# Kernel tuning notes

Measured on AMD Instinct MI355X. Metric: run time of the kernel, lower is better.

Reference implementation:

```python
import jax, jax.numpy as jnp
import numpy as np
import math

N_HEADS = 8
D_EMBED = 512
D_CROSS = 768
D_HEAD = D_EMBED // N_HEADS


def _conv1x1(w, b, t):
    # 1x1 conv == pointwise matmul over channel dim. t: [B, Cin, H, W], w: [Cout, Cin]
    out = jnp.einsum('oc,bchw->bohw', w, t)
    return out + b[None, :, None, None]


def setup_inputs() -> dict:
    key = jax.random.key(0)
    ks = jax.random.split(key, 10)
    s = 0.02
    return {
        'x': jax.random.normal(ks[0], (8, D_EMBED, 32, 32), dtype=jnp.float32),
        'y': jax.random.normal(ks[1], (8, D_CROSS, 32, 32), dtype=jnp.float32),
        'w_q': jax.random.normal(ks[2], (D_EMBED, D_EMBED), dtype=jnp.float32) * s,
        'b_q': jnp.zeros((D_EMBED,), dtype=jnp.float32),
        'w_k': jax.random.normal(ks[3], (D_EMBED, D_CROSS), dtype=jnp.float32) * s,
        'b_k': jnp.zeros((D_EMBED,), dtype=jnp.float32),
        'w_v': jax.random.normal(ks[4], (D_EMBED, D_CROSS), dtype=jnp.float32) * s,
        'b_v': jnp.zeros((D_EMBED,), dtype=jnp.float32),
        'w_o': jax.random.normal(ks[5], (D_EMBED, D_EMBED), dtype=jnp.float32) * s,
        'b_o': jnp.zeros((D_EMBED,), dtype=jnp.float32),
    }


def reference(x, y, w_q, b_q, w_k, b_k, w_v, b_v, w_o, b_o):
    B, C, H, W = x.shape
    N = H * W
    q = _conv1x1(w_q, b_q, x)  # [B, C, H, W]
    k = _conv1x1(w_k, b_k, y)
    v = _conv1x1(w_v, b_v, y)
    # flat reshape [B, C, H, W] -> [B, nH, d_head, N] (row-major, matches torch .view)
    q = q.reshape(B, N_HEADS, D_HEAD, N)
    k = k.reshape(B, N_HEADS, D_HEAD, N)
    v = v.reshape(B, N_HEADS, D_HEAD, N)
    # attn = q^T k / sqrt(d_head): [B, nH, N, N]
    scores = jnp.einsum('bhdq,bhdk->bhqk', q, k) / math.sqrt(D_HEAD)
    attn = jax.nn.softmax(scores, axis=-1)
    # out = attn @ v^T : [B, nH, N, d_head]
    out = jnp.einsum('bhqk,bhdk->bhqd', attn, v)
    # faithful quirk: flat reshape (no transpose back) to [B, C, H, W]
    out = out.reshape(B, N_HEADS * D_HEAD, H, W)
    return _conv1x1(w_o, b_o, out)
```

## Files before the change

### kernel.cpp

```cpp
#include <hip/hip_runtime.h>
#include <cstddef>
#include <cstdint>


typedef short bs8 __attribute__((ext_vector_type(8)));
typedef short bs4 __attribute__((ext_vector_type(4)));
typedef float fx4 __attribute__((ext_vector_type(4)));

#define MFMA16(a, b, c) __builtin_amdgcn_mfma_f32_16x16x32_bf16((a), (b), (c), 0, 0, 0)

#define GLOAD_LDS16(g, l)                                                  \
  __builtin_amdgcn_global_load_lds(                                        \
      (const __attribute__((address_space(1))) void*)(g),                  \
      (__attribute__((address_space(3))) void*)(l), 16, 0, 0)

__device__ __forceinline__ short f2b(float f) {
  unsigned u = __builtin_bit_cast(unsigned, f);
  u = (u + 0x7fff + ((u >> 16) & 1)) >> 16;
  return (short)u;
}

__device__ __forceinline__ unsigned cvt_pk_bf16(float lo, float hi) {
  unsigned r;
  asm("v_cvt_pk_bf16_f32 %0, %1, %2" : "=v"(r) : "v"(lo), "v"(hi));
  return r;
}

__device__ __forceinline__ float exp2_fast(float x) {
  float r;
  asm("v_exp_f32 %0, %1" : "=v"(r) : "v"(x));
  return r;
}

#define QSCALE 0.1803368801111244f

__global__ __launch_bounds__(256) void prep(
    const float* __restrict__ w_q, const float* __restrict__ w_k,
    const float* __restrict__ w_v, const float* __restrict__ w_o,
    short* __restrict__ wdst,
    const float* __restrict__ x, short* __restrict__ xt,
    const float* __restrict__ y, short* __restrict__ yt)
{
  __shared__ short T[64][72];
  const int bid = blockIdx.x;
  const int t = threadIdx.x;

  if (bid < 1280) {
    const int i = bid * 1024 + t * 4;
    const float* src; int off;
    if (i < 262144)       { src = w_q; off = 0; }
    else if (i < 655360)  { src = w_k; off = 262144; }
    else if (i < 1048576) { src = w_v; off = 655360; }
    else                  { src = w_o; off = 1048576; }
    float4 f = *(const float4*)(src + (i - off));
    bs4 o; o[0] = f2b(f.x); o[1] = f2b(f.y); o[2] = f2b(f.z); o[3] = f2b(f.w);
    *(bs4*)(wdst + i) = o;
    return;
  }

  const float* src; short* dst; int C, nt, ct, b;
  if (bid < 2304) {
    const int local = bid - 1280;
    src = x; dst = xt; C = 512;
    nt = local & 15; ct = (local >> 4) & 7; b = local >> 7;
  } else {
    const int local = bid - 2304;
    src = y; dst = yt; C = 768;
    nt = local & 15; const int rest = local >> 4; ct = rest % 12; b = rest / 12;
  }

  const size_t srcBase = ((size_t)b * C + ct * 64) * 1024 + nt * 64;
  #pragma unroll
  for (int p = 0; p < 4; ++p) {
    const int lin = p * 256 + t;
    const int row = lin >> 4;
    const int seg = lin & 15;
    float4 f = *(const float4*)(src + srcBase + (size_t)row * 1024 + seg * 4);
    T[seg * 4 + 0][row] = f2b(f.x);
    T[seg * 4 + 1][row] = f2b(f.y);
    T[seg * 4 + 2][row] = f2b(f.z);
    T[seg * 4 + 3][row] = f2b(f.w);
  }
  __syncthreads();
  const size_t dstBase = ((size_t)b * 1024 + nt * 64) * C + ct * 64;
  #pragma unroll
  for (int p = 0; p < 2; ++p) {
    const int lin = p * 256 + t;
    const int row = lin >> 3;
    const int seg = lin & 7;
    *(bs8*)(dst + dstBase + (size_t)row * C + seg * 8) = *(const bs8*)&T[row][seg * 8];
  }
}

__global__ __launch_bounds__(256) void tcast_b(
    const short* __restrict__ src, short* __restrict__ dst, int C)
{
  __shared__ short T[64][72];
  const int t = threadIdx.x;
  const int nt = blockIdx.x, ct = blockIdx.y, b = blockIdx.z;
  const size_t srcBase = ((size_t)b * C + ct * 64) * 1024 + nt * 64;
  #pragma unroll
  for (int p = 0; p < 4; ++p) {
    const int lin = p * 256 + t;
    const int row = lin >> 4;
    const int seg = lin & 15;
    bs4 v = *(const bs4*)(src + srcBase + (size_t)row * 1024 + seg * 4);
    #pragma unroll
    for (int j = 0; j < 4; ++j) T[seg * 4 + j][row] = v[j];
  }
  __syncthreads();
  const size_t dstBase = ((size_t)b * 1024 + nt * 64) * C + ct * 64;
  #pragma unroll
  for (int p = 0; p < 2; ++p) {
    const int lin = p * 256 + t;
    const int row = lin >> 3;
    const int seg = lin & 7;
    *(bs8*)(dst + dstBase + (size_t)row * C + seg * 8) = *(const bs8*)&T[row][seg * 8];
  }
}

template<int MODE, int MTL2>
__device__ __forceinline__ void gemm2_body(
    short* As0, short* As1, short* Bs0, short* Bs1, int hw, int tid,
    const short* __restrict__ W, const short* __restrict__ Xt,
    const float* __restrict__ bias, const float* __restrict__ bias2,
    void* __restrict__ Cout, void* __restrict__ Cout2, int K, float scale)
{
  const int wid = tid >> 6, l = tid & 63;
  const int swz = (hw & 7) * (8 << MTL2) + (hw >> 3);
  const int n0 = (swz & 7) * 128;
  const int m0 = ((swz >> 3) & ((1 << MTL2) - 1)) * 128;
  const int b  = swz >> (3 + MTL2);
  const int wm = wid >> 2, wn = wid & 3;

  const int lrow = l >> 3;
  const int swz8 = ((l & 7) ^ lrow) * 8;
  const int x7 = l & 7;

  const short* Wg = W + (size_t)m0 * K;
  const short* Xg = Xt + ((size_t)b * 1024 + n0) * K;

  fx4 acc[4][2] = {};
  const int NK = K >> 6;

  #pragma unroll
  for (int j = 0; j < 2; ++j) {
    const int rb = j * 64 + wid * 8;
    const int row = rb + lrow;
    GLOAD_LDS16(Wg + (size_t)row * K + swz8, As0 + rb * 64);
    GLOAD_LDS16(Xg + (size_t)row * K + swz8, Bs0 + rb * 64);
  }
  __syncthreads();

  auto gstep = [&](const short* AsC, const short* BsC, short* AsN, short* BsN,
                   int kn, bool pre) {
    if (pre) {
      #pragma unroll
      for (int j = 0; j < 2; ++j) {
        const int rb = j * 64 + wid * 8;
        const int row = rb + lrow;
        GLOAD_LDS16(Wg + (size_t)row * K + kn + swz8, AsN + rb * 64);
        GLOAD_LDS16(Xg + (size_t)row * K + kn + swz8, BsN + rb * 64);
      }
    }
    #pragma unroll
    for (int kb = 0; kb < 2; ++kb) {
      bs8 af[4], bfr[2];
      const int u = (kb * 4 + (l >> 4)) ^ x7;
      #pragma unroll
      for (int ms = 0; ms < 4; ++ms) {
        const int rr = wm * 64 + ms * 16 + (l & 15);
        af[ms] = *(const bs8*)&AsC[rr * 64 + u * 8];
      }
      #pragma unroll
      for (int ns = 0; ns < 2; ++ns) {
        const int rr = wn * 32 + ns * 16 + (l & 15);
        bfr[ns] = *(const bs8*)&BsC[rr * 64 + u * 8];
      }
      #pragma unroll
      for (int ms = 0; ms < 4; ++ms)
        #pragma unroll
        for (int ns = 0; ns < 2; ++ns)
          acc[ms][ns] = MFMA16(af[ms], bfr[ns], acc[ms][ns]);
    }
    __syncthreads();
  };

  const int NK2 = NK >> 1;
  for (int p = 0; p < NK2; ++p) {
    gstep(As0, Bs0, As1, Bs1, (2 * p + 1) * 64, true);
    gstep(As1, Bs1, As0, Bs0, (2 * p + 2) * 64, (2 * p + 2) < NK);
  }

  #pragma unroll
  for (int ms = 0; ms < 4; ++ms) {
    #pragma unroll
    for (int ns = 0; ns < 2; ++ns) {
      const int n = n0 + wn * 32 + ns * 16 + (l & 15);
      const int mb = m0 + wm * 64 + ms * 16 + (l >> 4) * 4;
      if (MODE == 0) {
        const float f0 = (acc[ms][ns][0] + bias[mb + 0]) * scale;
        const float f1 = (acc[ms][ns][1] + bias[mb + 1]) * scale;
        const float f2 = (acc[ms][ns][2] + bias[mb + 2]) * scale;
        const float f3 = (acc[ms][ns][3] + bias[mb + 3]) * scale;
        uint2 od; od.x = cvt_pk_bf16(f0, f1); od.y = cvt_pk_bf16(f2, f3);
        short* dst = (short*)Cout + (((size_t)b * 8 + (mb >> 6)) * 1024 + n) * 64 + (mb & 63);
        *(uint2*)dst = od;
      } else if (MODE == 2) {
        #pragma unroll
        for (int r = 0; r < 4; ++r)
          ((float*)Cout)[((size_t)b * 512 + mb + r) * 1024 + n] = acc[ms][ns][r] + bias[mb + r];
      } else {
        if (mb < 512) {
          const float f0 = acc[ms][ns][0] + bias[mb + 0];
          const float f1 = acc[ms][ns][1] + bias[mb + 1];
          const float f2 = acc[ms][ns][2] + bias[mb + 2];
          const float f3 = acc[ms][ns][3] + bias[mb + 3];
          uint2 od; od.x = cvt_pk_bf16(f0, f1); od.y = cvt_pk_bf16(f2, f3);
          short* dst = (short*)Cout + (((size_t)b * 8 + (mb >> 6)) * 1024 + n) * 64 + (mb & 63);
          *(uint2*)dst = od;
        } else {
          const int c = mb - 512;
          #pragma unroll
          for (int r = 0; r < 4; ++r)
            ((short*)Cout2)[((size_t)b * 512 + c + r) * 1024 + n] = f2b(acc[ms][ns][r] + bias2[c + r]);
        }
      }
    }
  }
}

__global__ __launch_bounds__(512) void gemm_qkv(
    const short* __restrict__ wq, const short* __restrict__ wkv,
    const short* __restrict__ xt, const short* __restrict__ yt,
    const float* __restrict__ b_q, const float* __restrict__ b_k,
    const float* __restrict__ b_v,
    short* __restrict__ Qw, short* __restrict__ Kw, short* __restrict__ Vw)
{
  __shared__ short As[2][128 * 64];
  __shared__ short Bs[2][128 * 64];
  if (blockIdx.x < 256)
    gemm2_body<0, 2>(As[0], As[1], Bs[0], Bs[1], blockIdx.x, threadIdx.x,
                     wq, xt, b_q, nullptr, (void*)Qw, nullptr, 512, QSCALE);
  else
    gemm2_body<3, 3>(As[0], As[1], Bs[0], Bs[1], blockIdx.x - 256, threadIdx.x,
                     wkv, yt, b_k, b_v, (void*)Kw, (void*)Vw, 768, 1.0f);
}

__global__ __launch_bounds__(512) void gemm_o(
    const short* __restrict__ wo, const short* __restrict__ Ot,
    const float* __restrict__ b_o, float* __restrict__ out)
{
  __shared__ short As[2][128 * 64];
  __shared__ short Bs[2][128 * 64];
  gemm2_body<2, 2>(As[0], As[1], Bs[0], Bs[1], blockIdx.x, threadIdx.x,
                   wo, Ot, b_o, nullptr, (void*)out, nullptr, 512, 1.0f);
}

__global__ __launch_bounds__(512) void attn_mfma(
    const short* __restrict__ Q, const short* __restrict__ Kt,
    const short* __restrict__ V, short* __restrict__ O)
{
  __shared__ short Ks[2][64 * 64];
  __shared__ short Vs[2][64 * 64];
  __shared__ short Ps[8][16 * 64];

  const int t = threadIdx.x, wid = t >> 6, l = t & 63;
  const int hw = blockIdx.x;
  const int swzb = (hw & 7) * 64 + (hw >> 3);
  const int qt = swzb & 7, h = (swzb >> 3) & 7, b = swzb >> 6;
  const int q0 = qt * 128 + wid * 16;
  const size_t bh = (size_t)b * 8 + h;

  const short* Qg = Q + (bh * 1024 + q0) * 64;
  const short* Kg = Kt + bh * 1024 * 64;
  const short* Vg = V + bh * 64 * 1024;

  const int g = l >> 4;
  const int q = l & 15;
  const int x7 = q & 7;
  const int lrow = l >> 3;
  const int swz8 = ((l & 7) ^ lrow) * 8;
  short* Pw = Ps[wid];

  const bs8 onesf = {0x3F80, 0x3F80, 0x3F80, 0x3F80, 0x3F80, 0x3F80, 0x3F80, 0x3F80};

  bs8 qf[2];
  #pragma unroll
  for (int db = 0; db < 2; ++db)
    qf[db] = *(const bs8*)(Qg + (size_t)q * 64 + db * 32 + g * 8);

  {
    const int row = wid * 8 + lrow;
    GLOAD_LDS16(Kg + (size_t)row * 64 + swz8, &Ks[0][wid * 8 * 64]);
    GLOAD_LDS16(Vg + (size_t)row * 1024 + swz8, &Vs[0][wid * 8 * 64]);
  }
  __syncthreads();

  fx4 oacc[4] = {};
  fx4 lacc = {};

  auto tile = [&](const short* KsC, const short* VsC, short* KsN, short* VsN,
                  int ktn, bool pre) {
    if (pre) {
      const int k0n = ktn * 64;
      const int row = wid * 8 + lrow;
      GLOAD_LDS16(Kg + (size_t)(k0n + row) * 64 + swz8, KsN + wid * 8 * 64);
      GLOAD_LDS16(Vg + (size_t)row * 1024 + k0n + swz8, VsN + wid * 8 * 64);
    }

    fx4 s[4] = {};
    __builtin_amdgcn_s_setprio(1);
    #pragma unroll
    for (int ks = 0; ks < 4; ++ks) {
      const int rr = ks * 16 + q;
      #pragma unroll
      for (int db = 0; db < 2; ++db) {
        bs8 kf = *(const bs8*)&KsC[rr * 64 + ((db * 4 + g) ^ x7) * 8];
        s[ks] = MFMA16(kf, qf[db], s[ks]);
      }
    }
    __builtin_amdgcn_s_setprio(0);

    #pragma unroll
    for (int ks = 0; ks < 4; ++ks)
      #pragma unroll
      for (int r = 0; r < 4; ++r)
        s[ks][r] = exp2_fast(s[ks][r]);

    #pragma unroll
    for (int ks = 0; ks < 4; ++ks) {
      uint2 pd;
      pd.x = cvt_pk_bf16(s[ks][0], s[ks][1]);
      pd.y = cvt_pk_bf16(s[ks][2], s[ks][3]);
      const int u16 = ks * 2 + (g >> 1);
      *(uint2*)&Pw[q * 64 + (u16 ^ x7) * 8 + (g & 1) * 4] = pd;
    }

    __builtin_amdgcn_s_setprio(1);
    #pragma unroll
    for (int kb = 0; kb < 2; ++kb) {
      const int u = kb * 4 + g;
      bs8 pf = *(const bs8*)&Pw[q * 64 + (u ^ x7) * 8];
      lacc = MFMA16(pf, onesf, lacc);
      #pragma unroll
      for (int ds = 0; ds < 4; ++ds) {
        const int d = ds * 16 + q;
        bs8 vf = *(const bs8*)&VsC[d * 64 + (u ^ x7) * 8];
        oacc[ds] = MFMA16(pf, vf, oacc[ds]);
      }
    }
    __builtin_amdgcn_s_setprio(0);
    __syncthreads();
  };

  #pragma unroll 1
  for (int p = 0; p < 8; ++p) {
    tile(Ks[0], Vs[0], Ks[1], Vs[1], 2 * p + 1, true);
    tile(Ks[1], Vs[1], Ks[0], Vs[0], 2 * p + 2, p < 7);
  }

  float linv[4];
  #pragma unroll
  for (int r = 0; r < 4; ++r) linv[r] = 1.f / lacc[r];
  short* Og = O + (bh * 1024 + q0) * 64;
  #pragma unroll
  for (int ds = 0; ds < 4; ++ds) {
    const int d = ds * 16 + q;
    #pragma unroll
    for (int r = 0; r < 4; ++r)
      Og[(size_t)(g * 4 + r) * 64 + d] = f2b(oacc[ds][r] * linv[r]);
  }
}

extern "C" void kernel_launch(void* const* d_in, const int* in_sizes, int n_in,
                              void* d_out, int out_size, void* d_ws, size_t ws_size,
                              hipStream_t stream) {
  const float* x   = (const float*)d_in[0];
  const float* y   = (const float*)d_in[1];
  const float* w_q = (const float*)d_in[2];
  const float* b_q = (const float*)d_in[3];
  const float* w_k = (const float*)d_in[4];
  const float* b_k = (const float*)d_in[5];
  const float* w_v = (const float*)d_in[6];
  const float* b_v = (const float*)d_in[7];
  const float* w_o = (const float*)d_in[8];
  const float* b_o = (const float*)d_in[9];

  char* ws = (char*)d_ws;
  const size_t MiB = 1u << 20;
  short* xt  = (short*)(ws);
  short* yt  = (short*)(ws + 8 * MiB);
  short* Qw  = (short*)(ws + 20 * MiB);
  short* Kw  = (short*)(ws + 28 * MiB);
  short* Vw  = (short*)(ws + 36 * MiB);
  short* Ow  = (short*)(ws + 44 * MiB);
  short* Ot  = (short*)(ws + 52 * MiB);
  short* wqb = (short*)(ws + 60 * MiB);
  short* wkb = wqb + 262144;
  short* wob = wkb + 786432;

  hipLaunchKernelGGL(prep, dim3(3840), dim3(256), 0, stream,
                     w_q, w_k, w_v, w_o, wqb, x, xt, y, yt);
  hipLaunchKernelGGL(gemm_qkv, dim3(768), dim3(512), 0, stream,
                     wqb, wkb, xt, yt, b_q, b_k, b_v, Qw, Kw, Vw);
  hipLaunchKernelGGL(attn_mfma, dim3(512), dim3(512), 0, stream, Qw, Kw, Vw, Ow);
  hipLaunchKernelGGL(tcast_b, dim3(16, 8, 8), dim3(256), 0, stream, Ow, Ot, 512);
  hipLaunchKernelGGL(gemm_o, dim3(256), dim3(512), 0, stream, wob, Ot, b_o, (float*)d_out);
}
```

Measured before the change: 79.56 us.

## Switch attention to 32x32 MFMA with register-resident P, dropping LDS roundtrip

The attention kernel now uses 32x32x16 bf16 MFMA. Each of 4 waves (256 threads) handles 32 query rows instead of 8 waves with 16 rows each. The exp'd scores are packed to bf16 and fed straight from registers as the A operand of the PV MFMA, which removes the per-wave LDS P buffer and its write/read traffic. The V fragments are now assembled from two 4-element LDS reads to match the 32x32 operand layout. The tradeoff is higher register pressure and fewer waves per block, so less latency hiding per block.

```diff
diff --git a/kernel.cpp b/kernel.cpp
--- a/kernel.cpp
+++ b/kernel.cpp
@@ -6,8 +6,11 @@
 typedef short bs8 __attribute__((ext_vector_type(8)));
 typedef short bs4 __attribute__((ext_vector_type(4)));
 typedef float fx4 __attribute__((ext_vector_type(4)));
+typedef float fx16 __attribute__((ext_vector_type(16)));
+typedef unsigned ux4 __attribute__((ext_vector_type(4)));
 
 #define MFMA16(a, b, c) __builtin_amdgcn_mfma_f32_16x16x32_bf16((a), (b), (c), 0, 0, 0)
+#define MFMA32(a, b, c) __builtin_amdgcn_mfma_f32_32x32x16_bf16((a), (b), (c), 0, 0, 0)
 
 #define GLOAD_LDS16(g, l)                                                  \
   __builtin_amdgcn_global_load_lds(                                        \
@@ -257,99 +260,101 @@
                    wo, Ot, b_o, nullptr, (void*)out, nullptr, 512, 1.0f);
 }
 
-__global__ __launch_bounds__(512) void attn_mfma(
+__global__ __launch_bounds__(256) void attn_mfma(
     const short* __restrict__ Q, const short* __restrict__ Kt,
     const short* __restrict__ V, short* __restrict__ O)
 {
   __shared__ short Ks[2][64 * 64];
   __shared__ short Vs[2][64 * 64];
-  __shared__ short Ps[8][16 * 64];
 
   const int t = threadIdx.x, wid = t >> 6, l = t & 63;
   const int hw = blockIdx.x;
   const int swzb = (hw & 7) * 64 + (hw >> 3);
   const int qt = swzb & 7, h = (swzb >> 3) & 7, b = swzb >> 6;
-  const int q0 = qt * 128 + wid * 16;
+  const int q0w = qt * 128 + wid * 32;
   const size_t bh = (size_t)b * 8 + h;
 
-  const short* Qg = Q + (bh * 1024 + q0) * 64;
+  const short* Qg = Q + (bh * 1024 + q0w) * 64;
   const short* Kg = Kt + bh * 1024 * 64;
   const short* Vg = V + bh * 64 * 1024;
 
-  const int g = l >> 4;
-  const int q = l & 15;
-  const int x7 = q & 7;
+  const int l31 = l & 31, hi = l >> 5, x7 = l & 7;
   const int lrow = l >> 3;
   const int swz8 = ((l & 7) ^ lrow) * 8;
-  short* Pw = Ps[wid];
-
-  const bs8 onesf = {0x3F80, 0x3F80, 0x3F80, 0x3F80, 0x3F80, 0x3F80, 0x3F80, 0x3F80};
-
-  bs8 qf[2];
-  #pragma unroll
-  for (int db = 0; db < 2; ++db)
-    qf[db] = *(const bs8*)(Qg + (size_t)q * 64 + db * 32 + g * 8);
-
-  {
-    const int row = wid * 8 + lrow;
-    GLOAD_LDS16(Kg + (size_t)row * 64 + swz8, &Ks[0][wid * 8 * 64]);
-    GLOAD_LDS16(Vg + (size_t)row * 1024 + swz8, &Vs[0][wid * 8 * 64]);
+
+  const bs8 onesf = {0x3F80, 0x3F80, 0x3F80, 0x3F80,
+                     0x3F80, 0x3F80, 0x3F80, 0x3F80};
+
+  bs8 qf[4];
+  #pragma unroll
+  for (int ks = 0; ks < 4; ++ks)
+    qf[ks] = *(const bs8*)(Qg + (size_t)l31 * 64 + ks * 16 + hi * 8);
+
+  #pragma unroll
+  for (int p = 0; p < 2; ++p) {
+    const int rb = p * 32 + wid * 8;
+    GLOAD_LDS16(Kg + (size_t)(rb + lrow) * 64 + swz8, &Ks[0][rb * 64]);
+    GLOAD_LDS16(Vg + (size_t)(rb + lrow) * 1024 + swz8, &Vs[0][rb * 64]);
   }
   __syncthreads();
 
-  fx4 oacc[4] = {};
-  fx4 lacc = {};
+  fx16 oacc[2] = {};
+  fx16 lacc = {};
 
   auto tile = [&](const short* KsC, const short* VsC, short* KsN, short* VsN,
                   int ktn, bool pre) {
     if (pre) {
       const int k0n = ktn * 64;
-      const int row = wid * 8 + lrow;
-      GLOAD_LDS16(Kg + (size_t)(k0n + row) * 64 + swz8, KsN + wid * 8 * 64);
-      GLOAD_LDS16(Vg + (size_t)row * 1024 + k0n + swz8, VsN + wid * 8 * 64);
-    }
-
-    fx4 s[4] = {};
+      #pragma unroll
+      for (int p = 0; p < 2; ++p) {
+        const int rb = p * 32 + wid * 8;
+        GLOAD_LDS16(Kg + (size_t)(k0n + rb + lrow) * 64 + swz8, KsN + rb * 64);
+        GLOAD_LDS16(Vg + (size_t)(rb + lrow) * 1024 + k0n + swz8, VsN + rb * 64);
+      }
+    }
+
+    fx16 s0 = {}, s1 = {};
     __builtin_amdgcn_s_setprio(1);
     #pragma unroll
     for (int ks = 0; ks < 4; ++ks) {
-      const int rr = ks * 16 + q;
+      bs8 kf = *(const bs8*)&KsC[l31 * 64 + ((ks * 2 + hi) ^ x7) * 8];
+      s0 = MFMA32(kf, qf[ks], s0);
+    }
+    #pragma unroll
+    for (int ks = 0; ks < 4; ++ks) {
+      bs8 kf = *(const bs8*)&KsC[(32 + l31) * 64 + ((ks * 2 + hi) ^ x7) * 8];
+      s1 = MFMA32(kf, qf[ks], s1);
+    }
+    __builtin_amdgcn_s_setprio(0);
+
+    #pragma unroll
+    for (int r = 0; r < 16; ++r) s0[r] = exp2_fast(s0[r]);
+    #pragma unroll
+    for (int r = 0; r < 16; ++r) s1[r] = exp2_fast(s1[r]);
+
+    unsigned U0[8], U1[8];
+    #pragma unroll
+    for (int u = 0; u < 8; ++u) {
+      U0[u] = cvt_pk_bf16(s0[2 * u], s0[2 * u + 1]);
+      U1[u] = cvt_pk_bf16(s1[2 * u], s1[2 * u + 1]);
+    }
+
+    __builtin_amdgcn_s_setprio(1);
+    auto pvstep = [&](const unsigned* Us, int si) {
+      const int base = (si & 1) * 4;
+      ux4 pw = {Us[base], Us[base + 1], Us[base + 2], Us[base + 3]};
+      bs8 pf = __builtin_bit_cast(bs8, pw);
+      lacc = MFMA32(pf, onesf, lacc);
       #pragma unroll
       for (int db = 0; db < 2; ++db) {
-        bs8 kf = *(const bs8*)&KsC[rr * 64 + ((db * 4 + g) ^ x7) * 8];
-        s[ks] = MFMA16(kf, qf[db], s[ks]);
-      }
-    }
-    __builtin_amdgcn_s_setprio(0);
-
-    #pragma unroll
-    for (int ks = 0; ks < 4; ++ks)
-      #pragma unroll
-      for (int r = 0; r < 4; ++r)
-        s[ks][r] = exp2_fast(s[ks][r]);
-
-    #pragma unroll
-    for (int ks = 0; ks < 4; ++ks) {
-      uint2 pd;
-      pd.x = cvt_pk_bf16(s[ks][0], s[ks][1]);
-      pd.y = cvt_pk_bf16(s[ks][2], s[ks][3]);
-      const int u16 = ks * 2 + (g >> 1);
-      *(uint2*)&Pw[q * 64 + (u16 ^ x7) * 8 + (g & 1) * 4] = pd;
-    }
-
-    __builtin_amdgcn_s_setprio(1);
-    #pragma unroll
-    for (int kb = 0; kb < 2; ++kb) {
-      const int u = kb * 4 + g;
-      bs8 pf = *(const bs8*)&Pw[q * 64 + (u ^ x7) * 8];
-      lacc = MFMA16(pf, onesf, lacc);
-      #pragma unroll
-      for (int ds = 0; ds < 4; ++ds) {
-        const int d = ds * 16 + q;
-        bs8 vf = *(const bs8*)&VsC[d * 64 + (u ^ x7) * 8];
-        oacc[ds] = MFMA16(pf, vf, oacc[ds]);
-      }
-    }
+        const int d = db * 32 + l31;
+        bs4 v0 = *(const bs4*)&VsC[d * 64 + ((si * 2 + 0) ^ x7) * 8 + hi * 4];
+        bs4 v1 = *(const bs4*)&VsC[d * 64 + ((si * 2 + 1) ^ x7) * 8 + hi * 4];
+        bs8 vf = {v0[0], v0[1], v0[2], v0[3], v1[0], v1[1], v1[2], v1[3]};
+        oacc[db] = MFMA32(pf, vf, oacc[db]);
+      }
+    };
+    pvstep(U0, 0); pvstep(U0, 1); pvstep(U1, 2); pvstep(U1, 3);
     __builtin_amdgcn_s_setprio(0);
     __syncthreads();
   };
@@ -360,17 +365,17 @@
     tile(Ks[1], Vs[1], Ks[0], Vs[0], 2 * p + 2, p < 7);
   }
 
-  float linv[4];
-  #pragma unroll
-  for (int r = 0; r < 4; ++r) linv[r] = 1.f / lacc[r];
-  short* Og = O + (bh * 1024 + q0) * 64;
-  #pragma unroll
-  for (int ds = 0; ds < 4; ++ds) {
-    const int d = ds * 16 + q;
-    #pragma unroll
-    for (int r = 0; r < 4; ++r)
-      Og[(size_t)(g * 4 + r) * 64 + d] = f2b(oacc[ds][r] * linv[r]);
-  }
+  float linv[16];
+  #pragma unroll
+  for (int r = 0; r < 16; ++r) linv[r] = 1.f / lacc[r];
+  short* Og = O + (bh * 1024 + q0w) * 64;
+  #pragma unroll
+  for (int db = 0; db < 2; ++db)
+    #pragma unroll
+    for (int r = 0; r < 16; ++r) {
+      const int qlocal = (r & 3) + 8 * (r >> 2) + 4 * hi;
+      Og[(size_t)qlocal * 64 + db * 32 + l31] = f2b(oacc[db][r] * linv[r]);
+    }
 }
 
 extern "C" void kernel_launch(void* const* d_in, const int* in_sizes, int n_in,
@@ -404,7 +409,7 @@
                      w_q, w_k, w_v, w_o, wqb, x, xt, y, yt);
   hipLaunchKernelGGL(gemm_qkv, dim3(768), dim3(512), 0, stream,
                      wqb, wkb, xt, yt, b_q, b_k, b_v, Qw, Kw, Vw);
-  hipLaunchKernelGGL(attn_mfma, dim3(512), dim3(512), 0, stream, Qw, Kw, Vw, Ow);
+  hipLaunchKernelGGL(attn_mfma, dim3(512), dim3(256), 0, stream, Qw, Kw, Vw, Ow);
   hipLaunchKernelGGL(tcast_b, dim3(16, 8, 8), dim3(256), 0, stream, Ow, Ot, 512);
   hipLaunchKernelGGL(gemm_o, dim3(256), dim3(512), 0, stream, wob, Ot, b_o, (float*)d_out);
 }
```

New measurement: 82.29 us. 1.03x slower.

## Fuse output transpose into attention epilogue, drop tcast_b kernel

Applied to the files above, without the earlier changes.

The attention kernel now stages its normalized bf16 output in shared memory and writes it directly in the transposed token-major layout that gemm_o consumes. This removes the separate tcast_b launch and its extra global read and write of the attention output. The cost is an extra shared-memory staging pass with two block barriers in the attention epilogue, plus strided 16-byte global stores.

```diff
diff --git a/kernel.cpp b/kernel.cpp
--- a/kernel.cpp
+++ b/kernel.cpp
@@ -6,6 +6,7 @@
 typedef short bs8 __attribute__((ext_vector_type(8)));
 typedef short bs4 __attribute__((ext_vector_type(4)));
 typedef float fx4 __attribute__((ext_vector_type(4)));
+typedef unsigned ux4 __attribute__((ext_vector_type(4)));
 
 #define MFMA16(a, b, c) __builtin_amdgcn_mfma_f32_16x16x32_bf16((a), (b), (c), 0, 0, 0)
 
@@ -80,33 +81,6 @@
     T[seg * 4 + 1][row] = f2b(f.y);
     T[seg * 4 + 2][row] = f2b(f.z);
     T[seg * 4 + 3][row] = f2b(f.w);
-  }
-  __syncthreads();
-  const size_t dstBase = ((size_t)b * 1024 + nt * 64) * C + ct * 64;
-  #pragma unroll
-  for (int p = 0; p < 2; ++p) {
-    const int lin = p * 256 + t;
-    const int row = lin >> 3;
-    const int seg = lin & 7;
-    *(bs8*)(dst + dstBase + (size_t)row * C + seg * 8) = *(const bs8*)&T[row][seg * 8];
-  }
-}
-
-__global__ __launch_bounds__(256) void tcast_b(
-    const short* __restrict__ src, short* __restrict__ dst, int C)
-{
-  __shared__ short T[64][72];
-  const int t = threadIdx.x;
-  const int nt = blockIdx.x, ct = blockIdx.y, b = blockIdx.z;
-  const size_t srcBase = ((size_t)b * C + ct * 64) * 1024 + nt * 64;
-  #pragma unroll
-  for (int p = 0; p < 4; ++p) {
-    const int lin = p * 256 + t;
-    const int row = lin >> 4;
-    const int seg = lin & 15;
-    bs4 v = *(const bs4*)(src + srcBase + (size_t)row * 1024 + seg * 4);
-    #pragma unroll
-    for (int j = 0; j < 4; ++j) T[seg * 4 + j][row] = v[j];
   }
   __syncthreads();
   const size_t dstBase = ((size_t)b * 1024 + nt * 64) * C + ct * 64;
@@ -259,7 +233,7 @@
 
 __global__ __launch_bounds__(512) void attn_mfma(
     const short* __restrict__ Q, const short* __restrict__ Kt,
-    const short* __restrict__ V, short* __restrict__ O)
+    const short* __restrict__ V, short* __restrict__ Ot)
 {
   __shared__ short Ks[2][64 * 64];
   __shared__ short Vs[2][64 * 64];
@@ -283,7 +257,8 @@
   const int swz8 = ((l & 7) ^ lrow) * 8;
   short* Pw = Ps[wid];
 
-  const bs8 onesf = {0x3F80, 0x3F80, 0x3F80, 0x3F80, 0x3F80, 0x3F80, 0x3F80, 0x3F80};
+  const bs8 onesf = {0x3F80, 0x3F80, 0x3F80, 0x3F80,
+                     0x3F80, 0x3F80, 0x3F80, 0x3F80};
 
   bs8 qf[2];
   #pragma unroll
@@ -360,16 +335,26 @@
     tile(Ks[1], Vs[1], Ks[0], Vs[0], 2 * p + 2, p < 7);
   }
 
+  __syncthreads();
+  short* Sq = &Ps[0][0];
   float linv[4];
   #pragma unroll
   for (int r = 0; r < 4; ++r) linv[r] = 1.f / lacc[r];
-  short* Og = O + (bh * 1024 + q0) * 64;
   #pragma unroll
   for (int ds = 0; ds < 4; ++ds) {
     const int d = ds * 16 + q;
     #pragma unroll
-    for (int r = 0; r < 4; ++r)
-      Og[(size_t)(g * 4 + r) * 64 + d] = f2b(oacc[ds][r] * linv[r]);
+    for (int r = 0; r < 4; ++r) {
+      const int tok = (g * 4 + r) * 64 + d;
+      Sq[tok * 8 + wid] = f2b(oacc[ds][r] * linv[r]);
+    }
+  }
+  __syncthreads();
+  short* OtB = Ot + ((size_t)b * 1024) * 512 + h * 64 + qt * 8;
+  #pragma unroll
+  for (int rr = 0; rr < 2; ++rr) {
+    const int tok = rr * 512 + t;
+    *(ux4*)(OtB + (size_t)tok * 512) = *(const ux4*)&Sq[tok * 8];
   }
 }
 
@@ -394,7 +379,6 @@
   short* Qw  = (short*)(ws + 20 * MiB);
   short* Kw  = (short*)(ws + 28 * MiB);
   short* Vw  = (short*)(ws + 36 * MiB);
-  short* Ow  = (short*)(ws + 44 * MiB);
   short* Ot  = (short*)(ws + 52 * MiB);
   short* wqb = (short*)(ws + 60 * MiB);
   short* wkb = wqb + 262144;
@@ -404,7 +388,6 @@
                      w_q, w_k, w_v, w_o, wqb, x, xt, y, yt);
   hipLaunchKernelGGL(gemm_qkv, dim3(768), dim3(512), 0, stream,
                      wqb, wkb, xt, yt, b_q, b_k, b_v, Qw, Kw, Vw);
-  hipLaunchKernelGGL(attn_mfma, dim3(512), dim3(512), 0, stream, Qw, Kw, Vw, Ow);
-  hipLaunchKernelGGL(tcast_b, dim3(16, 8, 8), dim3(256), 0, stream, Ow, Ot, 512);
+  hipLaunchKernelGGL(attn_mfma, dim3(512), dim3(512), 0, stream, Qw, Kw, Vw, Ot);
   hipLaunchKernelGGL(gemm_o, dim3(256), dim3(512), 0, stream, wob, Ot, b_o, (float*)d_out);
 }
```

Measured after the change: 75.86 us. 4.7% less time.
